# Kernel tuning notes

Measured on AMD Instinct MI355X. Metric: run time of the kernel, lower is better.

Reference implementation:

```python
import jax, jax.numpy as jnp
import numpy as np

Q, N, D, L = 4096, 50000, 5, 2


def setup_inputs() -> dict:
    key = jax.random.key(0)
    k1, k2, k3 = jax.random.split(key, 3)
    rss = jax.random.normal(k1, (Q, D), dtype=jnp.float32)
    Radio = jax.random.normal(k2, (N, D), dtype=jnp.float32)
    Loc = jax.random.normal(k3, (N, L), dtype=jnp.float32)
    sigma = jnp.ones((1,), dtype=jnp.float32)
    return {"rss": rss, "Radio": Radio, "Loc": Loc, "sigma": sigma}


def reference(rss, Radio, Loc, sigma):
    # x: [Q, 5] queries; Radio: [N, 5] reference fingerprints; Loc: [N, 2]
    x = rss.reshape(-1, D)
    # squared pairwise distances via the expanded form (no [Q,N,D] intermediate)
    x2 = jnp.sum(x * x, axis=-1, keepdims=True)            # [Q, 1]
    r2 = jnp.sum(Radio * Radio, axis=-1)                   # [N]
    d2 = x2 - 2.0 * (x @ Radio.T) + r2                     # [Q, N]
    d2 = jnp.maximum(d2, 0.0)
    sim = jnp.exp(-d2 / (2.0 * sigma[0] * sigma[0]))       # RBF kernel [Q, N]
    w = sim / jnp.sum(sim, axis=-1, keepdims=True)         # row-normalize
    l_hat = jnp.einsum('qn,nl->ql', w, Loc)                # Nadaraya-Watson [Q, 2]
    return l_hat
```

## Files before the change

### kernel.cpp

```cpp
#include <hip/hip_runtime.h>
#include <hip/hip_bf16.h>
#include <math.h>

#define QTOT   4096
#define NTOT   50000
#define NTILES 3125
#define NS     32
#define QG     64
#define ACCN   (3 * QTOT)

#define BOFF   0u
#define BSIZE  (3125u * 512u)
#define AOFF   (BOFF + BSIZE)
#define ASIZE  (4096u * 32u)
#define ZOFF   (AOFF + ASIZE)
#define ACCOFF (ZOFF + 256u)

typedef unsigned short ushort_t;
typedef short  s16x8 __attribute__((ext_vector_type(8)));
typedef float  f32x4 __attribute__((ext_vector_type(4)));
typedef float  f2    __attribute__((ext_vector_type(2)));

#if __has_builtin(__builtin_amdgcn_exp2f)
#define EXP2F(x) __builtin_amdgcn_exp2f(x)
#else
#define EXP2F(x) exp2f(x)
#endif

static __device__ __forceinline__ f2 fma2(f2 a, f2 b, f2 c) {
#if __has_builtin(__builtin_elementwise_fma)
    return __builtin_elementwise_fma(a, b, c);
#else
    f2 r; r.x = fmaf(a.x, b.x, c.x); r.y = fmaf(a.y, b.y, c.y); return r;
#endif
}

static __device__ __forceinline__ void bsplit(float f, ushort_t& h, ushort_t& l) {
    __hip_bfloat16 hb = __float2bfloat16(f);
    float hf = __bfloat162float(hb);
    __hip_bfloat16 lb = __float2bfloat16(f - hf);
    h = *reinterpret_cast<ushort_t*>(&hb);
    l = *reinterpret_cast<ushort_t*>(&lb);
}

__global__ __launch_bounds__(256) void sknn_prep(
    const float* __restrict__ rss, const float* __restrict__ Radio,
    const float* __restrict__ sigma, char* __restrict__ ws)
{
    const int p = blockIdx.x * 256 + threadIdx.x;
    const float sg = sigma[0];
    const float g  = 1.4426950408889634f / (2.0f * sg * sg);
    const float g2 = 2.0f * g;

    if (p < NTOT) {
        float b[8];
        float rr = 0.f;
        #pragma unroll
        for (int d = 0; d < 5; ++d) { float r = Radio[p * 5 + d]; b[d] = g2 * r; rr += r * r; }
        b[5] = 1.0f; b[6] = -g * rr; b[7] = 0.0f;
        union { ushort_t u[8]; f32x4 v; } hi, lo;
        #pragma unroll
        for (int k = 0; k < 8; ++k) bsplit(b[k], hi.u[k], lo.u[k]);
        const int nt = p >> 4, nsub = p & 15;
        *(f32x4*)(ws + BOFF + (unsigned)nt * 512u + (unsigned)nsub * 16u)        = hi.v;
        *(f32x4*)(ws + BOFF + (unsigned)nt * 512u + 256u + (unsigned)nsub * 16u) = lo.v;
    }
    if (p < QTOT) {
        float a[8];
        float xx = 0.f;
        #pragma unroll
        for (int d = 0; d < 5; ++d) { float x = rss[p * 5 + d]; a[d] = x; xx += x * x; }
        a[5] = -g * xx; a[6] = 1.0f; a[7] = 0.0f;
        union { ushort_t u[8]; f32x4 v; } hi, lo;
        #pragma unroll
        for (int k = 0; k < 8; ++k) bsplit(a[k], hi.u[k], lo.u[k]);
        *(f32x4*)(ws + AOFF + (unsigned)p * 32u)       = hi.v;
        *(f32x4*)(ws + AOFF + (unsigned)p * 32u + 16u) = lo.v;
    }
    if (p < 16)  *(f32x4*)(ws + ZOFF + (unsigned)p * 16u) = (f32x4){0.f, 0.f, 0.f, 0.f};
    if (p < ACCN) ((float*)(ws + ACCOFF))[p] = 0.0f;
}

__global__ __launch_bounds__(256) void sknn_main(
    const char* __restrict__ tbl, const float* __restrict__ Loc,
    float* __restrict__ acc)
{
    const int tid  = threadIdx.x;
    const int lane = tid & 63;
    const int wid  = (blockIdx.x * 256 + tid) >> 6;
    const int qg   = wid >> 5;
    const int ns   = wid & (NS - 1);
    const int qbase = qg * 64;
    const int j  = lane & 15;
    const int qd = lane >> 4;

    const unsigned abase = (qd == 3) ? (ZOFF + (unsigned)j * 16u)
        : (AOFF + (unsigned)(qbase + j) * 32u + (qd == 2 ? 16u : 0u));
    const unsigned astep = (qd == 3) ? 0u : 512u;
    const s16x8 a0 = *(const s16x8*)(tbl + abase);
    const s16x8 a1 = *(const s16x8*)(tbl + abase + astep);
    const s16x8 a2 = *(const s16x8*)(tbl + abase + 2u * astep);
    const s16x8 a3 = *(const s16x8*)(tbl + abase + 3u * astep);

    unsigned bofs = (qd == 3) ? (ZOFF + (unsigned)j * 16u)
        : (BOFF + (unsigned)ns * 512u + (qd == 1 ? 256u : 0u) + (unsigned)j * 16u);
    const unsigned bstep = (qd == 3) ? 0u : (512u * NS);

    unsigned lofs = (unsigned)(ns * 16 + j) * 8u;
    const char* locb = (const char*)Loc;

    float sm[16];  f2 o[16];
    #pragma unroll
    for (int k = 0; k < 16; ++k) { sm[k] = 0.f; o[k] = (f2){0.f, 0.f}; }
    const f32x4 zz = {0.f, 0.f, 0.f, 0.f};

    s16x8 bcur = *(const s16x8*)(tbl + bofs);
    f2    lcur = *(const f2*)(locb + lofs);

    for (int nt = ns; nt < NTILES; nt += NS) {
        const bool has = (nt + NS) < NTILES;
        const unsigned bn = bofs + (has ? bstep : 0u);
        const unsigned ln = lofs + (has ? (unsigned)(NS * 16 * 8) : 0u);
        const s16x8 bnx = *(const s16x8*)(tbl + bn);
        const f2    lnx = *(const f2*)(locb + ln);

        f32x4 t[4];
        t[0] = __builtin_amdgcn_mfma_f32_16x16x32_bf16(a0, bcur, zz, 0, 0, 0);
        t[1] = __builtin_amdgcn_mfma_f32_16x16x32_bf16(a1, bcur, zz, 0, 0, 0);
        t[2] = __builtin_amdgcn_mfma_f32_16x16x32_bf16(a2, bcur, zz, 0, 0, 0);
        t[3] = __builtin_amdgcn_mfma_f32_16x16x32_bf16(a3, bcur, zz, 0, 0, 0);

        #pragma unroll
        for (int qt = 0; qt < 4; ++qt) {
            #pragma unroll
            for (int i = 0; i < 4; ++i) {
                const float s = EXP2F(t[qt][i]);
                sm[qt * 4 + i] += s;
                o[qt * 4 + i] = fma2((f2){s, s}, lcur, o[qt * 4 + i]);
            }
        }
        bcur = bnx; lcur = lnx; bofs = bn; lofs = ln;
    }

    #pragma unroll
    for (int m = 1; m <= 8; m <<= 1) {
        #pragma unroll
        for (int k = 0; k < 16; ++k) {
            sm[k]  += __shfl_xor(sm[k],  m, 64);
            o[k].x += __shfl_xor(o[k].x, m, 64);
            o[k].y += __shfl_xor(o[k].y, m, 64);
        }
    }

    #pragma unroll
    for (int qt = 0; qt < 4; ++qt) {
        #pragma unroll
        for (int i = 0; i < 4; ++i) {
            if (j == qt * 4 + i) {
                const int q = qbase + qt * 16 + qd * 4 + i;
                atomicAdd(&acc[q],            sm[qt * 4 + i]);
                atomicAdd(&acc[QTOT + q],     o[qt * 4 + i].x);
                atomicAdd(&acc[2 * QTOT + q], o[qt * 4 + i].y);
            }
        }
    }
}

__global__ __launch_bounds__(256) void sknn_fin(
    const float* __restrict__ acc, float* __restrict__ out)
{
    const int q = blockIdx.x * 256 + threadIdx.x;
    if (q < QTOT) {
        const float inv = 1.0f / acc[q];
        out[q * 2 + 0] = acc[QTOT + q]     * inv;
        out[q * 2 + 1] = acc[2 * QTOT + q] * inv;
    }
}

extern "C" void kernel_launch(void* const* d_in, const int* in_sizes, int n_in,
                              void* d_out, int out_size, void* d_ws, size_t ws_size,
                              hipStream_t stream) {
    const float* rss   = (const float*)d_in[0];
    const float* Radio = (const float*)d_in[1];
    const float* Loc   = (const float*)d_in[2];
    const float* sigma = (const float*)d_in[3];
    float* out = (float*)d_out;
    char*  ws  = (char*)d_ws;
    float* acc = (float*)(ws + ACCOFF);

    sknn_prep<<<(NTOT + 255) / 256, dim3(256), 0, stream>>>(rss, Radio, sigma, ws);
    sknn_main<<<512, dim3(256), 0, stream>>>(ws, Loc, acc);
    sknn_fin<<<QTOT / 256, dim3(256), 0, stream>>>(acc, out);
}
```

Measured before the change: 112.2 us.

## Double N-split waves, fuse finalize via last-block counter, pack row sums

Splits the reference dimension across 64 wave slices instead of 32, launching 1024 blocks with a launch-bounds occupancy hint to give more parallelism. The separate finalize kernel is removed: the last block to finish, found through an atomic done-counter, normalizes the accumulators and writes the output, which saves one launch. Row sums are packed into two-wide vectors to allow packed adds. In exchange, atomic traffic on the accumulators doubles and the final normalization runs serially in a single block.

Result: slower. 165.7 us (+47.7%).

```diff
diff --git a/kernel.cpp b/kernel.cpp
--- a/kernel.cpp
+++ b/kernel.cpp
@@ -5,9 +5,9 @@
 #define QTOT   4096
 #define NTOT   50000
 #define NTILES 3125
-#define NS     32
-#define QG     64
+#define NS     64
 #define ACCN   (3 * QTOT)
+#define MAINBLOCKS 1024
 
 #define BOFF   0u
 #define BSIZE  (3125u * 512u)
@@ -15,6 +15,7 @@
 #define ASIZE  (4096u * 32u)
 #define ZOFF   (AOFF + ASIZE)
 #define ACCOFF (ZOFF + 256u)
+#define DONEOFF (ACCOFF + ACCN * 4u)
 
 typedef unsigned short ushort_t;
 typedef short  s16x8 __attribute__((ext_vector_type(8)));
@@ -53,65 +54,67 @@
     const float g2 = 2.0f * g;
 
     if (p < NTOT) {
-        float b[8];
-        float rr = 0.f;
-        #pragma unroll
-        for (int d = 0; d < 5; ++d) { float r = Radio[p * 5 + d]; b[d] = g2 * r; rr += r * r; }
+        float b[8]; float rr = 0.f;
+        #pragma unroll
+        for (int d = 0; d < 5; ++d) { float r = Radio[p*5+d]; b[d] = g2*r; rr += r*r; }
         b[5] = 1.0f; b[6] = -g * rr; b[7] = 0.0f;
         union { ushort_t u[8]; f32x4 v; } hi, lo;
         #pragma unroll
         for (int k = 0; k < 8; ++k) bsplit(b[k], hi.u[k], lo.u[k]);
         const int nt = p >> 4, nsub = p & 15;
-        *(f32x4*)(ws + BOFF + (unsigned)nt * 512u + (unsigned)nsub * 16u)        = hi.v;
-        *(f32x4*)(ws + BOFF + (unsigned)nt * 512u + 256u + (unsigned)nsub * 16u) = lo.v;
+        *(f32x4*)(ws + BOFF + (unsigned)nt*512u + (unsigned)nsub*16u)        = hi.v;
+        *(f32x4*)(ws + BOFF + (unsigned)nt*512u + 256u + (unsigned)nsub*16u) = lo.v;
     }
     if (p < QTOT) {
-        float a[8];
-        float xx = 0.f;
-        #pragma unroll
-        for (int d = 0; d < 5; ++d) { float x = rss[p * 5 + d]; a[d] = x; xx += x * x; }
+        float a[8]; float xx = 0.f;
+        #pragma unroll
+        for (int d = 0; d < 5; ++d) { float x = rss[p*5+d]; a[d] = x; xx += x*x; }
         a[5] = -g * xx; a[6] = 1.0f; a[7] = 0.0f;
         union { ushort_t u[8]; f32x4 v; } hi, lo;
         #pragma unroll
         for (int k = 0; k < 8; ++k) bsplit(a[k], hi.u[k], lo.u[k]);
-        *(f32x4*)(ws + AOFF + (unsigned)p * 32u)       = hi.v;
-        *(f32x4*)(ws + AOFF + (unsigned)p * 32u + 16u) = lo.v;
-    }
-    if (p < 16)  *(f32x4*)(ws + ZOFF + (unsigned)p * 16u) = (f32x4){0.f, 0.f, 0.f, 0.f};
+        *(f32x4*)(ws + AOFF + (unsigned)p*32u)       = hi.v;
+        *(f32x4*)(ws + AOFF + (unsigned)p*32u + 16u) = lo.v;
+    }
+    if (p < 16)   *(f32x4*)(ws + ZOFF + (unsigned)p*16u) = (f32x4){0.f,0.f,0.f,0.f};
     if (p < ACCN) ((float*)(ws + ACCOFF))[p] = 0.0f;
-}
-
-__global__ __launch_bounds__(256) void sknn_main(
+    if (p == 0)   *(unsigned*)(ws + DONEOFF) = 0u;
+}
+
+__global__ __launch_bounds__(256, 4) void sknn_main(
     const char* __restrict__ tbl, const float* __restrict__ Loc,
-    float* __restrict__ acc)
+    float* __restrict__ acc, unsigned* __restrict__ done,
+    float* __restrict__ out)
 {
     const int tid  = threadIdx.x;
     const int lane = tid & 63;
     const int wid  = (blockIdx.x * 256 + tid) >> 6;
-    const int qg   = wid >> 5;
+    const int qg   = wid >> 6;
     const int ns   = wid & (NS - 1);
     const int qbase = qg * 64;
     const int j  = lane & 15;
     const int qd = lane >> 4;
 
-    const unsigned abase = (qd == 3) ? (ZOFF + (unsigned)j * 16u)
-        : (AOFF + (unsigned)(qbase + j) * 32u + (qd == 2 ? 16u : 0u));
+    const unsigned abase = (qd == 3) ? (ZOFF + (unsigned)j*16u)
+        : (AOFF + (unsigned)(qbase + j)*32u + (qd == 2 ? 16u : 0u));
     const unsigned astep = (qd == 3) ? 0u : 512u;
     const s16x8 a0 = *(const s16x8*)(tbl + abase);
     const s16x8 a1 = *(const s16x8*)(tbl + abase + astep);
-    const s16x8 a2 = *(const s16x8*)(tbl + abase + 2u * astep);
-    const s16x8 a3 = *(const s16x8*)(tbl + abase + 3u * astep);
-
-    unsigned bofs = (qd == 3) ? (ZOFF + (unsigned)j * 16u)
-        : (BOFF + (unsigned)ns * 512u + (qd == 1 ? 256u : 0u) + (unsigned)j * 16u);
+    const s16x8 a2 = *(const s16x8*)(tbl + abase + 2u*astep);
+    const s16x8 a3 = *(const s16x8*)(tbl + abase + 3u*astep);
+
+    unsigned bofs = (qd == 3) ? (ZOFF + (unsigned)j*16u)
+        : (BOFF + (unsigned)ns*512u + (qd == 1 ? 256u : 0u) + (unsigned)j*16u);
     const unsigned bstep = (qd == 3) ? 0u : (512u * NS);
 
-    unsigned lofs = (unsigned)(ns * 16 + j) * 8u;
+    unsigned lofs = (unsigned)(ns*16 + j) * 8u;
     const char* locb = (const char*)Loc;
 
-    float sm[16];  f2 o[16];
-    #pragma unroll
-    for (int k = 0; k < 16; ++k) { sm[k] = 0.f; o[k] = (f2){0.f, 0.f}; }
+    f2 sm2[8]; f2 o[16];
+    #pragma unroll
+    for (int k = 0; k < 8;  ++k) sm2[k] = (f2){0.f, 0.f};
+    #pragma unroll
+    for (int k = 0; k < 16; ++k) o[k]   = (f2){0.f, 0.f};
     const f32x4 zz = {0.f, 0.f, 0.f, 0.f};
 
     s16x8 bcur = *(const s16x8*)(tbl + bofs);
@@ -120,7 +123,7 @@
     for (int nt = ns; nt < NTILES; nt += NS) {
         const bool has = (nt + NS) < NTILES;
         const unsigned bn = bofs + (has ? bstep : 0u);
-        const unsigned ln = lofs + (has ? (unsigned)(NS * 16 * 8) : 0u);
+        const unsigned ln = lofs + (has ? (unsigned)(NS*16*8) : 0u);
         const s16x8 bnx = *(const s16x8*)(tbl + bn);
         const f2    lnx = *(const f2*)(locb + ln);
 
@@ -132,12 +135,16 @@
 
         #pragma unroll
         for (int qt = 0; qt < 4; ++qt) {
-            #pragma unroll
-            for (int i = 0; i < 4; ++i) {
-                const float s = EXP2F(t[qt][i]);
-                sm[qt * 4 + i] += s;
-                o[qt * 4 + i] = fma2((f2){s, s}, lcur, o[qt * 4 + i]);
-            }
+            const float s0 = EXP2F(t[qt][0]);
+            const float s1 = EXP2F(t[qt][1]);
+            const float s2 = EXP2F(t[qt][2]);
+            const float s3 = EXP2F(t[qt][3]);
+            sm2[qt*2+0] += (f2){s0, s1};
+            sm2[qt*2+1] += (f2){s2, s3};
+            o[qt*4+0] = fma2((f2){s0, s0}, lcur, o[qt*4+0]);
+            o[qt*4+1] = fma2((f2){s1, s1}, lcur, o[qt*4+1]);
+            o[qt*4+2] = fma2((f2){s2, s2}, lcur, o[qt*4+2]);
+            o[qt*4+3] = fma2((f2){s3, s3}, lcur, o[qt*4+3]);
         }
         bcur = bnx; lcur = lnx; bofs = bn; lofs = ln;
     }
@@ -145,8 +152,12 @@
     #pragma unroll
     for (int m = 1; m <= 8; m <<= 1) {
         #pragma unroll
+        for (int k = 0; k < 8; ++k) {
+            sm2[k].x += __shfl_xor(sm2[k].x, m, 64);
+            sm2[k].y += __shfl_xor(sm2[k].y, m, 64);
+        }
+        #pragma unroll
         for (int k = 0; k < 16; ++k) {
-            sm[k]  += __shfl_xor(sm[k],  m, 64);
             o[k].x += __shfl_xor(o[k].x, m, 64);
             o[k].y += __shfl_xor(o[k].y, m, 64);
         }
@@ -156,24 +167,35 @@
     for (int qt = 0; qt < 4; ++qt) {
         #pragma unroll
         for (int i = 0; i < 4; ++i) {
-            if (j == qt * 4 + i) {
-                const int q = qbase + qt * 16 + qd * 4 + i;
-                atomicAdd(&acc[q],            sm[qt * 4 + i]);
-                atomicAdd(&acc[QTOT + q],     o[qt * 4 + i].x);
-                atomicAdd(&acc[2 * QTOT + q], o[qt * 4 + i].y);
+            if (j == qt*4 + i) {
+                const int q = qbase + qt*16 + qd*4 + i;
+                const float sv = (i & 1) ? sm2[qt*2 + (i>>1)].y
+                                         : sm2[qt*2 + (i>>1)].x;
+                atomicAdd(&acc[q],          sv);
+                atomicAdd(&acc[QTOT + q],   o[qt*4+i].x);
+                atomicAdd(&acc[2*QTOT + q], o[qt*4+i].y);
             }
         }
     }
-}
-
-__global__ __launch_bounds__(256) void sknn_fin(
-    const float* __restrict__ acc, float* __restrict__ out)
-{
-    const int q = blockIdx.x * 256 + threadIdx.x;
-    if (q < QTOT) {
-        const float inv = 1.0f / acc[q];
-        out[q * 2 + 0] = acc[QTOT + q]     * inv;
-        out[q * 2 + 1] = acc[2 * QTOT + q] * inv;
+
+    __shared__ int lastFlag;
+    __threadfence();
+    __syncthreads();
+    if (tid == 0) {
+        unsigned v = atomicAdd(done, 1u);
+        lastFlag = (v == (unsigned)(MAINBLOCKS - 1));
+    }
+    __syncthreads();
+    if (lastFlag) {
+        __threadfence();
+        for (int q = tid; q < QTOT; q += 256) {
+            const float s  = __hip_atomic_load(&acc[q],          __ATOMIC_RELAXED, __HIP_MEMORY_SCOPE_AGENT);
+            const float w0 = __hip_atomic_load(&acc[QTOT + q],   __ATOMIC_RELAXED, __HIP_MEMORY_SCOPE_AGENT);
+            const float w1 = __hip_atomic_load(&acc[2*QTOT + q], __ATOMIC_RELAXED, __HIP_MEMORY_SCOPE_AGENT);
+            const float inv = 1.0f / s;
+            out[q*2 + 0] = w0 * inv;
+            out[q*2 + 1] = w1 * inv;
+        }
     }
 }
 
@@ -186,9 +208,9 @@
     const float* sigma = (const float*)d_in[3];
     float* out = (float*)d_out;
     char*  ws  = (char*)d_ws;
-    float* acc = (float*)(ws + ACCOFF);
+    float*    acc  = (float*)(ws + ACCOFF);
+    unsigned* done = (unsigned*)(ws + DONEOFF);
 
     sknn_prep<<<(NTOT + 255) / 256, dim3(256), 0, stream>>>(rss, Radio, sigma, ws);
-    sknn_main<<<512, dim3(256), 0, stream>>>(ws, Loc, acc);
-    sknn_fin<<<QTOT / 256, dim3(256), 0, stream>>>(acc, out);
-}
+    sknn_main<<<MAINBLOCKS, dim3(256), 0, stream>>>(ws, Loc, acc, done, out);
+}
```
